# Performance work log

Measured on AMD Instinct MI355X. Metric: run time of the kernel, lower is better.

Reference implementation:

```python
import jax, jax.numpy as jnp
import numpy as np
from jax import lax

K = 4
OUT_PLANES = 128
TEMPERATURE = 30.0


def setup_inputs() -> dict:
    key = jax.random.key(0)
    ks = jax.random.split(key, 5)
    in_planes, k = 128, 3
    he_std = float(np.sqrt(2.0)) * (in_planes * k * k) ** (-0.5)
    return {
        "x": jax.random.normal(ks[0], (16, in_planes, 64, 64), jnp.float32),
        "weight": jax.random.normal(ks[1], (K * OUT_PLANES, in_planes, k, k), jnp.float32) * he_std,
        "bias": jax.random.normal(ks[2], (K * OUT_PLANES,), jnp.float32) * 0.01,
        "se_w1": jax.random.normal(ks[3], (33, in_planes), jnp.float32) * (2.0 / 33) ** 0.5,
        "se_w2": jax.random.normal(ks[4], (K, 33), jnp.float32) * (2.0 / K) ** 0.5,
        "se_b2": jnp.zeros((K,), jnp.float32),
    }


def reference(x, weight, bias, se_w1, se_w2, se_b2):
    B = x.shape[0]
    # SE attention: global avg pool -> fc1 -> relu -> fc2 -> softmax(./T)
    pooled = x.mean(axis=(2, 3))                      # [B, Cin]
    h = jax.nn.relu(pooled @ se_w1.T)                 # [B, hidden]
    logits = h @ se_w2.T + se_b2                      # [B, K]
    attn = jax.nn.softmax(logits / TEMPERATURE, axis=1)
    # conv with K*out channels (groups=1, stride=1, pad=1, dil=1)
    y = lax.conv_general_dilated(
        x, weight, window_strides=(1, 1), padding=[(1, 1), (1, 1)],
        dimension_numbers=("NCHW", "OIHW", "NCHW"))
    y = y + bias[None, :, None, None]                 # [B, K*out, Ho, Wo]
    Ho, Wo = y.shape[2], y.shape[3]
    y = y.reshape(B, K, OUT_PLANES, Ho, Wo)
    # attention-weighted combine over K branches (bmm in torch)
    return jnp.einsum("bk,bkohw->bohw", attn, y)
```

## Files before the change

kernel.cpp:

```cpp
#include <hip/hip_runtime.h>
#include <cstdint>
#include <cstddef>

typedef unsigned short u16;
typedef __attribute__((ext_vector_type(8))) short short8;
typedef __attribute__((ext_vector_type(4))) float f32x4;

__device__ __forceinline__ u16 f2bf(float f){
  union { float f; unsigned u; } c; c.f = f;
  unsigned u = c.u;
  u += 0x7fffu + ((u >> 16) & 1u);
  return (u16)(u >> 16);
}
__device__ __forceinline__ unsigned pk2(float a, float b){
  union { float f; unsigned u; } ca, cb; ca.f = a; cb.f = b;
  return ((ca.u + 0x8000u) >> 16) | ((cb.u + 0x8000u) & 0xFFFF0000u);
}

#define XB_STRIDE 557568
#define XR_STRIDE 8448


#define GLD_LDS(gsrc, ldst) \
  __builtin_amdgcn_global_load_lds((const __attribute__((address_space(1))) void*)(gsrc), \
                                   (__attribute__((address_space(3))) void*)(ldst), 16, 0, 0)

__global__ __launch_bounds__(256) void xpose_pool(
    const float* __restrict__ x, u16* __restrict__ xT2, float* __restrict__ part)
{
  const int bid = blockIdx.x;
  const int b = bid & 15, chunk = bid >> 4;
  const int pos0 = chunk << 7;
  const int tid = threadIdx.x;
  __shared__ u16 tile[16384];
  __shared__ float psum[128 * 33];
  const float* xb = x + ((size_t)b << 19) + pos0;
  const int p4 = (tid & 31) << 2;
  const int swz = (tid & 31) & 7;

  if (chunk == 0){
    u16* xh = xT2 + (size_t)b * XB_STRIDE;
    for (int i = tid; i < 4160; i += 256){
      const int p = i >> 4, oct = i & 15;
      int row, col;
      if (p < 66)      { row = 0;        col = p; }
      else if (p < 132){ row = 65;       col = p - 66; }
      else if (p < 196){ row = p - 131;  col = 0; }
      else             { row = p - 195;  col = 65; }
      *(uint4*)(xh + row * XR_STRIDE + (col << 7) + (oct << 3)) =
          make_uint4(0u, 0u, 0u, 0u);
    }
  }

  #pragma unroll
  for (int i = 0; i < 2; ++i){
    const int gci = (tid >> 5) + (i << 3);
    const int ci8 = gci << 3;
    float4 L[8];
    #pragma unroll
    for (int j = 0; j < 8; ++j)
      L[j] = *(const float4*)(xb + ((size_t)(ci8 + j) << 12) + p4);
    #pragma unroll
    for (int j = 0; j < 8; ++j)
      psum[(ci8 + j) * 33 + (tid & 31)] = L[j].x + L[j].y + L[j].z + L[j].w;
    const int gs = gci ^ swz;
    const float* e = (const float*)L;
    #pragma unroll
    for (int p = 0; p < 4; ++p){
      const int row = p4 + p;
      uint4 V;
      V.x = pk2(e[0 * 4 + p], e[1 * 4 + p]);
      V.y = pk2(e[2 * 4 + p], e[3 * 4 + p]);
      V.z = pk2(e[4 * 4 + p], e[5 * 4 + p]);
      V.w = pk2(e[6 * 4 + p], e[7 * 4 + p]);
      *(uint4*)(tile + (row << 7) + (gs << 3)) = V;
    }
  }
  __syncthreads();

  if (tid < 128){
    float s = 0.f;
    #pragma unroll 8
    for (int j = 0; j < 32; ++j) s += psum[tid * 33 + j];
    part[((b << 5) + chunk) * 128 + tid] = s;
  }

  u16* xo = xT2 + (size_t)b * XB_STRIDE;
  const int g = tid & 15, rb = (tid >> 4) << 3;
  #pragma unroll
  for (int r = 0; r < 8; ++r){
    const int row = rb + r;
    const int gs = g ^ ((row >> 2) & 7);
    uint4 v = *(const uint4*)(tile + (row << 7) + (gs << 3));
    const int pos = pos0 + row;
    const int h = pos >> 6, w = pos & 63;
    *(uint4*)(xo + (h + 1) * XR_STRIDE + ((w + 1) << 7) + (g << 3)) = v;
  }
}

__global__ __launch_bounds__(256) void combine(
    const float* __restrict__ W, const float* __restrict__ bias,
    const float* __restrict__ part, const float* __restrict__ w1,
    const float* __restrict__ w2, const float* __restrict__ b2,
    u16* __restrict__ wcomb, float* __restrict__ bcomb)
{
  __shared__ float wlds[9216];
  __shared__ float sp[128];
  __shared__ float sh[33];
  __shared__ float sat[4];
  const int bid = blockIdx.x;
  const int b = bid & 15, cp = bid >> 4;
  const int tid = threadIdx.x;

  #pragma unroll
  for (int it = 0; it < 9; ++it){
    const int G = it * 256 + tid;
    const int k = G / 576, rem = G - k * 576;
    const int co_l = rem / 288, j4 = rem - co_l * 288;
    const float* src = W + (size_t)(k * 128 + (cp << 1) + co_l) * 1152 + (j4 << 2);
    GLD_LDS(src, (char*)wlds + (G << 4));
  }

  if (tid < 128){
    const float* pb = part + (b << 12);
    float s = 0.f;
    #pragma unroll 8
    for (int c = 0; c < 32; ++c) s += pb[(c << 7) + tid];
    sp[tid] = s * (1.f / 4096.f);
  }
  __syncthreads();
  if (tid < 33){
    float h = 0.f;
    for (int ci = 0; ci < 128; ++ci) h += sp[ci] * w1[tid * 128 + ci];
    sh[tid] = fmaxf(h, 0.f);
  }
  __syncthreads();
  if (tid == 0){
    float l[4];
    #pragma unroll
    for (int t = 0; t < 4; ++t){
      float v = b2[t];
      for (int j = 0; j < 33; ++j) v += sh[j] * w2[t * 33 + j];
      l[t] = v * (1.f / 30.f);
    }
    float m = fmaxf(fmaxf(l[0], l[1]), fmaxf(l[2], l[3]));
    float e0 = __expf(l[0] - m), e1 = __expf(l[1] - m);
    float e2 = __expf(l[2] - m), e3 = __expf(l[3] - m);
    float inv = 1.f / (e0 + e1 + e2 + e3);
    sat[0] = e0 * inv; sat[1] = e1 * inv; sat[2] = e2 * inv; sat[3] = e3 * inv;
  }
  asm volatile("s_waitcnt vmcnt(0)" ::: "memory");
  __syncthreads();
  const float a0 = sat[0], a1 = sat[1], a2 = sat[2], a3 = sat[3];

  if (tid < 2){
    const int co = (cp << 1) + tid;
    bcomb[(b << 7) + co] = a0 * bias[co] + a1 * bias[128 + co]
                         + a2 * bias[256 + co] + a3 * bias[384 + co];
  }

  u16* wob = wcomb + (size_t)b * 147456;
  for (int gi = tid; gi < 288; gi += 256){
    const int co_l = gi / 144;
    const int r = gi - co_l * 144;
    const int tap = r >> 4;
    const int gg = r & 15;
    const int cq = gg >> 2, g = gg & 3;
    const int co = (cp << 1) + co_l;
    union { u16 h[8]; uint4 v; } pk;
    #pragma unroll
    for (int e = 0; e < 8; ++e){
      const int ci = (cq << 5) + (g << 3) + e;
      const int j = ci * 9 + tap;
      float s = a0 * wlds[co_l * 1152 + j]        + a1 * wlds[2304 + co_l * 1152 + j]
              + a2 * wlds[4608 + co_l * 1152 + j] + a3 * wlds[6912 + co_l * 1152 + j];
      pk.h[e] = f2bf(s);
    }
    *(uint4*)(wob + (((tap << 2) + cq) << 12) + (co << 5) + (g << 3)) = pk.v;
  }
}

__global__ __launch_bounds__(256, 2) void conv_mfma(
    const u16* __restrict__ xT2, const u16* __restrict__ wcomb,
    const float* __restrict__ bcomb, float* __restrict__ out)
{
  extern __shared__ char smem[];
  u16* s_x = (u16*)smem;
  u16* s_w = (u16*)(smem + 33792);

  const int tid = threadIdx.x;
  const int lane = tid & 63, wid = tid >> 6;
  const int wr = wid & 1, wcv = wid >> 1;
  const int l15 = lane & 15, hi = lane >> 4;

  const int bid = blockIdx.x;
  const int b = bid & 15;
  const int h0 = (bid >> 4) << 1;

  const u16* Abase = wcomb + (size_t)b * 147456;
  const u16* Xbase = xT2 + (size_t)b * XB_STRIDE;

#define STAGE_X(HF) { \
    _Pragma("unroll") \
    for (int _it = 0; _it < 9; ++_it){ \
      const int _G = _it * 256 + tid; \
      if (_it < 8 || _G < 2112){ \
        const int _slot = _G & 7, _t = _G >> 3; \
        const int _col = _t % 66, _row = _t / 66; \
        const u16* _src = Xbase + (h0 + _row) * XR_STRIDE + (_col << 7) \
                        + ((HF) << 6) + ((_slot ^ ((_col & 1) << 2)) << 3); \
        GLD_LDS(_src, s_x + (_G << 3)); \
      } \
    } }

#define STAGE_W(HF, TAP, BUF) { \
    const u16* _As = Abase + ((((TAP) << 2) + ((HF) << 1)) << 12); \
    u16* _sw = s_w + (BUF) * 8192; \
    _Pragma("unroll") \
    for (int _it = 0; _it < 4; ++_it){ \
      const int _G = _it * 256 + tid; \
      GLD_LDS(_As + (_G << 3), _sw + (_G << 3)); \
    } }

#define COMPUTE(TAP, BUF) { \
    const int _dh = (TAP) / 3, _dw = (TAP) - 3 * (_dh); \
    const u16* _sw = s_w + (BUF) * 8192; \
    _Pragma("unroll") \
    for (int _ks = 0; _ks < 2; ++_ks){ \
      short8 _af[4], _bf[4]; \
      _Pragma("unroll") \
      for (int _a = 0; _a < 4; ++_a){ \
        const int _co = (wcv << 6) + (_a << 4) + l15; \
        _af[_a] = *(const short8*)(_sw + (_ks << 12) + (_co << 5) + (hi << 3)); \
      } \
      _Pragma("unroll") \
      for (int _p = 0; _p < 4; ++_p){ \
        const int _col = l15 + _dw + (_p << 4); \
        const int _sl = ((_ks << 2) + hi) ^ ((_col & 1) << 2); \
        _bf[_p] = *(const short8*)(s_x + ((((wr + _dh) * 66 + _col) << 6) + (_sl << 3))); \
      } \
      _Pragma("unroll") \
      for (int _a = 0; _a < 4; ++_a) \
        _Pragma("unroll") \
        for (int _p = 0; _p < 4; ++_p) \
          acc[_a][_p] = __builtin_amdgcn_mfma_f32_16x16x32_bf16(_af[_a], _bf[_p], acc[_a][_p], 0, 0, 0); \
    } }

#define VM0_BAR { asm volatile("s_waitcnt vmcnt(0)" ::: "memory"); __syncthreads(); }

  f32x4 acc[4][4] = {};

  STAGE_X(0);
  STAGE_W(0, 0, 0);
  VM0_BAR;

  int buf = 0;
  for (int hf = 0; hf < 2; ++hf){
    #pragma unroll
    for (int tap = 0; tap < 9; ++tap){
      if (!(hf == 1 && tap == 8)){
        const int nh = (tap == 8) ? 1 : hf;
        const int nt = (tap == 8) ? 0 : tap + 1;
        STAGE_W(nh, nt, buf ^ 1);
      }
      COMPUTE(tap, buf);
      VM0_BAR;
      buf ^= 1;
      if (tap == 8 && hf == 0){
        STAGE_X(1);
        VM0_BAR;
      }
    }
  }

#undef VM0_BAR
#undef COMPUTE
#undef STAGE_W
#undef STAGE_X

  const int hrow = h0 + wr;
  float* ob = out + ((size_t)b << 19) + (hrow << 6) + l15;
  #pragma unroll
  for (int a = 0; a < 4; ++a){
    const int co0 = (wcv << 6) + (a << 4) + (hi << 2);
    #pragma unroll
    for (int r = 0; r < 4; ++r){
      const float bc = bcomb[(b << 7) + co0 + r];
      float* op = ob + (size_t)(co0 + r) * 4096;
      #pragma unroll
      for (int p = 0; p < 4; ++p)
        __builtin_nontemporal_store(acc[a][p][r] + bc, op + (p << 4));
    }
  }
}

extern "C" void kernel_launch(void* const* d_in, const int* in_sizes, int n_in,
                              void* d_out, int out_size, void* d_ws, size_t ws_size,
                              hipStream_t stream)
{
  const float* x    = (const float*)d_in[0];
  const float* W    = (const float*)d_in[1];
  const float* bias = (const float*)d_in[2];
  const float* w1   = (const float*)d_in[3];
  const float* w2   = (const float*)d_in[4];
  const float* b2   = (const float*)d_in[5];
  float* out = (float*)d_out;

  char* ws = (char*)d_ws;
  float* part  = (float*)(ws);
  float* bcomb = (float*)(ws + 262144);
  u16*   xT2   = (u16*)  (ws + 270592);
  u16*   wcomb = (u16*)  (ws + 18112768);

  xpose_pool<<<512, 256, 0, stream>>>(x, xT2, part);
  combine<<<1024, 256, 0, stream>>>(W, bias, part, w1, w2, b2, wcomb, bcomb);

  (void)hipFuncSetAttribute(reinterpret_cast<const void*>(conv_mfma),
                            hipFuncAttributeMaxDynamicSharedMemorySize, 66560);
  conv_mfma<<<512, 256, 66560, stream>>>(xT2, wcomb, bcomb, out);
}
```

Measured before the change: 50.33 us.

## Triple-buffer conv weights per 32-channel quarter and halve transpose block size

The conv kernel now splits input channels into four 32-wide quarters instead of two 64-wide halves. It keeps a three-slot weight ring, so stages run two taps ahead with partial vmcnt waits instead of a full drain before each barrier, and it raises wave priority around the MFMA block. LDS use drops, which should allow more blocks per CU, but there are more X restages and barriers. The transpose/pool kernel now uses 64-position chunks across 1024 blocks, and the combine kernel reduces over 64 partial sums.

```diff
diff --git a/kernel.cpp b/kernel.cpp
--- a/kernel.cpp
+++ b/kernel.cpp
@@ -25,18 +25,23 @@
   __builtin_amdgcn_global_load_lds((const __attribute__((address_space(1))) void*)(gsrc), \
                                    (__attribute__((address_space(3))) void*)(ldst), 16, 0, 0)
 
+#define BAR { asm volatile("s_waitcnt lgkmcnt(0)" ::: "memory"); \
+              __builtin_amdgcn_s_barrier(); }
+#define WAIT_VM(N) asm volatile("s_waitcnt vmcnt(" #N ")" ::: "memory")
+
 __global__ __launch_bounds__(256) void xpose_pool(
     const float* __restrict__ x, u16* __restrict__ xT2, float* __restrict__ part)
 {
   const int bid = blockIdx.x;
   const int b = bid & 15, chunk = bid >> 4;
-  const int pos0 = chunk << 7;
+  const int pos0 = chunk << 6;
   const int tid = threadIdx.x;
-  __shared__ u16 tile[16384];
-  __shared__ float psum[128 * 33];
+  __shared__ u16 tile[8192];
+  __shared__ float psum[128 * 17];
   const float* xb = x + ((size_t)b << 19) + pos0;
-  const int p4 = (tid & 31) << 2;
-  const int swz = (tid & 31) & 7;
+  const int rq = tid & 15;
+  const int p4 = rq << 2;
+  const int gci = tid >> 4;
 
   if (chunk == 0){
     u16* xh = xT2 + (size_t)b * XB_STRIDE;
@@ -52,9 +57,7 @@
     }
   }
 
-  #pragma unroll
-  for (int i = 0; i < 2; ++i){
-    const int gci = (tid >> 5) + (i << 3);
+  {
     const int ci8 = gci << 3;
     float4 L[8];
     #pragma unroll
@@ -62,8 +65,8 @@
       L[j] = *(const float4*)(xb + ((size_t)(ci8 + j) << 12) + p4);
     #pragma unroll
     for (int j = 0; j < 8; ++j)
-      psum[(ci8 + j) * 33 + (tid & 31)] = L[j].x + L[j].y + L[j].z + L[j].w;
-    const int gs = gci ^ swz;
+      psum[(ci8 + j) * 17 + rq] = L[j].x + L[j].y + L[j].z + L[j].w;
+    const int gs = gci ^ (rq & 7);
     const float* e = (const float*)L;
     #pragma unroll
     for (int p = 0; p < 4; ++p){
@@ -80,15 +83,15 @@
 
   if (tid < 128){
     float s = 0.f;
-    #pragma unroll 8
-    for (int j = 0; j < 32; ++j) s += psum[tid * 33 + j];
-    part[((b << 5) + chunk) * 128 + tid] = s;
+    #pragma unroll
+    for (int j = 0; j < 16; ++j) s += psum[tid * 17 + j];
+    part[(((b << 6) | chunk) << 7) + tid] = s;
   }
 
   u16* xo = xT2 + (size_t)b * XB_STRIDE;
-  const int g = tid & 15, rb = (tid >> 4) << 3;
+  const int g = tid & 15, rb = (tid >> 4) << 2;
   #pragma unroll
-  for (int r = 0; r < 8; ++r){
+  for (int r = 0; r < 4; ++r){
     const int row = rb + r;
     const int gs = g ^ ((row >> 2) & 7);
     uint4 v = *(const uint4*)(tile + (row << 7) + (gs << 3));
@@ -122,10 +125,10 @@
   }
 
   if (tid < 128){
-    const float* pb = part + (b << 12);
+    const float* pb = part + (b << 13);
     float s = 0.f;
     #pragma unroll 8
-    for (int c = 0; c < 32; ++c) s += pb[(c << 7) + tid];
+    for (int c = 0; c < 64; ++c) s += pb[(c << 7) + tid];
     sp[tid] = s * (1.f / 4096.f);
   }
   __syncthreads();
@@ -165,18 +168,18 @@
     const int r = gi - co_l * 144;
     const int tap = r >> 4;
     const int gg = r & 15;
-    const int cq = gg >> 2, g = gg & 3;
+    const int q = gg >> 2, g = gg & 3;
     const int co = (cp << 1) + co_l;
     union { u16 h[8]; uint4 v; } pk;
     #pragma unroll
     for (int e = 0; e < 8; ++e){
-      const int ci = (cq << 5) + (g << 3) + e;
+      const int ci = (q << 5) + (g << 3) + e;
       const int j = ci * 9 + tap;
       float s = a0 * wlds[co_l * 1152 + j]        + a1 * wlds[2304 + co_l * 1152 + j]
               + a2 * wlds[4608 + co_l * 1152 + j] + a3 * wlds[6912 + co_l * 1152 + j];
       pk.h[e] = f2bf(s);
     }
-    *(uint4*)(wob + (((tap << 2) + cq) << 12) + (co << 5) + (g << 3)) = pk.v;
+    *(uint4*)(wob + (((tap << 2) + q) << 12) + (co << 5) + (g << 3)) = pk.v;
   }
 }
 
@@ -186,7 +189,7 @@
 {
   extern __shared__ char smem[];
   u16* s_x = (u16*)smem;
-  u16* s_w = (u16*)(smem + 33792);
+  u16* s_w = (u16*)(smem + 16896);
 
   const int tid = threadIdx.x;
   const int lane = tid & 63, wid = tid >> 6;
@@ -200,80 +203,72 @@
   const u16* Abase = wcomb + (size_t)b * 147456;
   const u16* Xbase = xT2 + (size_t)b * XB_STRIDE;
 
-#define STAGE_X(HF) { \
+#define STAGE_X(Q) { \
     _Pragma("unroll") \
-    for (int _it = 0; _it < 9; ++_it){ \
+    for (int _it = 0; _it < 5; ++_it){ \
       const int _G = _it * 256 + tid; \
-      if (_it < 8 || _G < 2112){ \
-        const int _slot = _G & 7, _t = _G >> 3; \
+      if (_it < 4 || _G < 1056){ \
+        const int _oct = _G & 3, _t = _G >> 2; \
         const int _col = _t % 66, _row = _t / 66; \
         const u16* _src = Xbase + (h0 + _row) * XR_STRIDE + (_col << 7) \
-                        + ((HF) << 6) + ((_slot ^ ((_col & 1) << 2)) << 3); \
+                        + ((Q) << 5) + (_oct << 3); \
         GLD_LDS(_src, s_x + (_G << 3)); \
       } \
     } }
 
-#define STAGE_W(HF, TAP, BUF) { \
-    const u16* _As = Abase + ((((TAP) << 2) + ((HF) << 1)) << 12); \
-    u16* _sw = s_w + (BUF) * 8192; \
-    _Pragma("unroll") \
-    for (int _it = 0; _it < 4; ++_it){ \
-      const int _G = _it * 256 + tid; \
-      GLD_LDS(_As + (_G << 3), _sw + (_G << 3)); \
-    } }
+#define STAGE_W(Q, TAP, BUF) { \
+    const u16* _As = Abase + ((((TAP) << 2) + (Q)) << 12); \
+    u16* _sw = s_w + (BUF) * 4096; \
+    GLD_LDS(_As + (tid << 3), _sw + (tid << 3)); \
+    GLD_LDS(_As + ((tid + 256) << 3), _sw + ((tid + 256) << 3)); }
 
 #define COMPUTE(TAP, BUF) { \
     const int _dh = (TAP) / 3, _dw = (TAP) - 3 * (_dh); \
-    const u16* _sw = s_w + (BUF) * 8192; \
+    const u16* _sw = s_w + (BUF) * 4096; \
+    short8 _af[4], _bf[4]; \
     _Pragma("unroll") \
-    for (int _ks = 0; _ks < 2; ++_ks){ \
-      short8 _af[4], _bf[4]; \
+    for (int _a = 0; _a < 4; ++_a){ \
+      const int _co = (wcv << 6) + (_a << 4) + l15; \
+      _af[_a] = *(const short8*)(_sw + (_co << 5) + (hi << 3)); \
+    } \
+    _Pragma("unroll") \
+    for (int _p = 0; _p < 4; ++_p){ \
+      const int _col = l15 + _dw + (_p << 4); \
+      _bf[_p] = *(const short8*)(s_x + (((wr + _dh) * 66 + _col) << 5) + (hi << 3)); \
+    } \
+    _Pragma("unroll") \
+    for (int _a = 0; _a < 4; ++_a) \
       _Pragma("unroll") \
-      for (int _a = 0; _a < 4; ++_a){ \
-        const int _co = (wcv << 6) + (_a << 4) + l15; \
-        _af[_a] = *(const short8*)(_sw + (_ks << 12) + (_co << 5) + (hi << 3)); \
-      } \
-      _Pragma("unroll") \
-      for (int _p = 0; _p < 4; ++_p){ \
-        const int _col = l15 + _dw + (_p << 4); \
-        const int _sl = ((_ks << 2) + hi) ^ ((_col & 1) << 2); \
-        _bf[_p] = *(const short8*)(s_x + ((((wr + _dh) * 66 + _col) << 6) + (_sl << 3))); \
-      } \
-      _Pragma("unroll") \
-      for (int _a = 0; _a < 4; ++_a) \
-        _Pragma("unroll") \
-        for (int _p = 0; _p < 4; ++_p) \
-          acc[_a][_p] = __builtin_amdgcn_mfma_f32_16x16x32_bf16(_af[_a], _bf[_p], acc[_a][_p], 0, 0, 0); \
-    } }
-
-#define VM0_BAR { asm volatile("s_waitcnt vmcnt(0)" ::: "memory"); __syncthreads(); }
+      for (int _p = 0; _p < 4; ++_p) \
+        acc[_a][_p] = __builtin_amdgcn_mfma_f32_16x16x32_bf16(_af[_a], _bf[_p], acc[_a][_p], 0, 0, 0); }
 
   f32x4 acc[4][4] = {};
 
   STAGE_X(0);
   STAGE_W(0, 0, 0);
-  VM0_BAR;
-
-  int buf = 0;
-  for (int hf = 0; hf < 2; ++hf){
+  STAGE_W(0, 1, 1);
+
+  for (int q = 0; q < 4; ++q){
     #pragma unroll
     for (int tap = 0; tap < 9; ++tap){
-      if (!(hf == 1 && tap == 8)){
-        const int nh = (tap == 8) ? 1 : hf;
-        const int nt = (tap == 8) ? 0 : tap + 1;
-        STAGE_W(nh, nt, buf ^ 1);
+      if (tap == 8 && q == 3){ WAIT_VM(0); } else { WAIT_VM(2); }
+      BAR;
+      if (tap <= 6){
+        STAGE_W(q, tap + 2, (tap + 2) % 3);
+      } else if (tap == 7){
+        if (q < 3){ STAGE_W(q + 1, 0, 0); }
       }
-      COMPUTE(tap, buf);
-      VM0_BAR;
-      buf ^= 1;
-      if (tap == 8 && hf == 0){
-        STAGE_X(1);
-        VM0_BAR;
+      __builtin_amdgcn_s_setprio(1);
+      COMPUTE(tap, tap % 3);
+      __builtin_amdgcn_s_setprio(0);
+      if (tap == 8 && q < 3){
+        BAR;
+        STAGE_X(q + 1);
+        STAGE_W(q + 1, 1, 1);
       }
     }
   }
 
-#undef VM0_BAR
 #undef COMPUTE
 #undef STAGE_W
 #undef STAGE_X
@@ -308,14 +303,14 @@
 
   char* ws = (char*)d_ws;
   float* part  = (float*)(ws);
-  float* bcomb = (float*)(ws + 262144);
-  u16*   xT2   = (u16*)  (ws + 270592);
-  u16*   wcomb = (u16*)  (ws + 18112768);
-
-  xpose_pool<<<512, 256, 0, stream>>>(x, xT2, part);
+  float* bcomb = (float*)(ws + 524288);
+  u16*   xT2   = (u16*)  (ws + 532480);
+  u16*   wcomb = (u16*)  (ws + 18374656);
+
+  xpose_pool<<<1024, 256, 0, stream>>>(x, xT2, part);
   combine<<<1024, 256, 0, stream>>>(W, bias, part, w1, w2, b2, wcomb, bcomb);
 
   (void)hipFuncSetAttribute(reinterpret_cast<const void*>(conv_mfma),
-                            hipFuncAttributeMaxDynamicSharedMemorySize, 66560);
-  conv_mfma<<<512, 256, 66560, stream>>>(xT2, wcomb, bcomb, out);
-}
+                            hipFuncAttributeMaxDynamicSharedMemorySize, 41472);
+  conv_mfma<<<512, 256, 41472, stream>>>(xT2, wcomb, bcomb, out);
+}
```

Measured after the change: 49.27 us. 1.02x faster.
